# Kernel tuning notes

Hardware: AMD Instinct MI355X
Metric: run time of the kernel (lower is better)

Reference implementation:

```python
import jax, jax.numpy as jnp
import numpy as np

BS, SEQ, D_SSL = 256, 201, 1024
D1, D2 = 128, 64
N_NODE = SEQ // 3          # 67 nodes after max_pool1d(3)
N_POOL = int(N_NODE * 0.8) # 53 nodes after GraphPool(k=0.8)
EPS = 1e-5                 # BatchNorm eps (eval mode, running stats)


def setup_inputs() -> dict:
    key = jax.random.key(0)
    ks = jax.random.split(key, 16)
    def rn(k, shape, s=0.02):
        return jax.random.normal(k, shape, jnp.float32) * s
    return {
        "feat": jax.random.normal(ks[0], (BS, SEQ, D_SSL), jnp.float32),
        "W_ll": rn(ks[1], (D_SSL, D1)), "b_ll": jnp.zeros((D1,), jnp.float32),
        "bn1_g": jnp.ones((D1,), jnp.float32), "bn1_b": jnp.zeros((D1,), jnp.float32),
        "bn1_m": rn(ks[2], (D1,), 0.1),
        "bn1_v": jax.random.uniform(ks[3], (D1,), jnp.float32, 0.5, 1.5),
        "W_ap": rn(ks[4], (D1, D2)), "b_ap": jnp.zeros((D2,), jnp.float32),
        "att_w": rn(ks[5], (D2, 1), 0.1),
        "W_pa": rn(ks[6], (D1, D2)), "b_pa": jnp.zeros((D2,), jnp.float32),
        "W_pn": rn(ks[7], (D1, D2)), "b_pn": jnp.zeros((D2,), jnp.float32),
        "bn2_g": jnp.ones((D2,), jnp.float32), "bn2_b": jnp.zeros((D2,), jnp.float32),
        "bn2_m": rn(ks[8], (D2,), 0.1),
        "bn2_v": jax.random.uniform(ks[9], (D2,), jnp.float32, 0.5, 1.5),
        "W_pool": rn(ks[10], (D2, 1), 0.1), "b_pool": jnp.zeros((1,), jnp.float32),
        "W_proj": rn(ks[11], (D2, 1), 0.1), "b_proj": jnp.zeros((1,), jnp.float32),
        "W_node": rn(ks[12], (N_POOL, 2), 0.1), "b_node": jnp.zeros((2,), jnp.float32),
    }


def _bn(x, g, b, m, v):
    # eval-mode BatchNorm1d with running stats, applied per-channel (last dim)
    return (x - m) * jax.lax.rsqrt(v + EPS) * g + b


def reference(feat, W_ll, b_ll, bn1_g, bn1_b, bn1_m, bn1_v,
              W_ap, b_ap, att_w, W_pa, b_pa, W_pn, b_pn,
              bn2_g, bn2_b, bn2_m, bn2_v,
              W_pool, b_pool, W_proj, b_proj, W_node, b_node):
    # LL: (bs, seq, 1024) -> (bs, seq, 128)
    x = feat @ W_ll + b_ll
    # max_pool1d(kernel=3, stride=3) over the sequence dim -> (bs, 67, 128)
    x = x[:, :N_NODE * 3].reshape(BS, N_NODE, 3, D1).max(axis=2)
    x = jax.nn.selu(_bn(x, bn1_g, bn1_b, bn1_m, bn1_v))
    # --- GraphAttentionLayer ---
    pair = x[:, :, None, :] * x[:, None, :, :]            # (bs, n, n, 128) pairwise mul
    att = jnp.tanh(pair @ W_ap + b_ap) @ att_w            # (bs, n, n, 1)
    att = jax.nn.softmax(att, axis=-2)                    # softmax over second node axis
    x1 = jnp.einsum('bij,bjd->bid', att[..., 0], x) @ W_pa + b_pa
    x2 = x @ W_pn + b_pn
    h = jax.nn.selu(_bn(x1 + x2, bn2_g, bn2_b, bn2_m, bn2_v))  # (bs, n, 64)
    # --- GraphPool: top-k node selection ---
    scores = jax.nn.sigmoid(h @ W_pool + b_pool)          # (bs, n, 1)
    _, idx = jax.lax.top_k(scores[..., 0], N_POOL)        # (bs, 53)
    hs = jnp.take_along_axis(h * scores, idx[:, :, None], axis=1)  # (bs, 53, 64)
    # head: proj -> (bs, 53), proj_node -> (bs, 2)
    out = (hs @ W_proj + b_proj)[..., 0] @ W_node + b_node
    return out
```

## Files before the change

### kernel.cpp

```cpp
#include <hip/hip_runtime.h>
#include <stdint.h>
#include <math.h>


#define BS 256
#define SEQ 201
#define DS 1024
#define D1 128
#define D2 64
#define NN 67
#define NP 53
#define ROWS1 (BS * SEQ)
#define ROWS2 (BS * NN)

#define SELU_LAM 1.0507009873554805f
#define SELU_ALP 1.6732632423543772f

__device__ __forceinline__ float selu_f(float x) {
    return (x > 0.0f) ? SELU_LAM * x : SELU_LAM * (SELU_ALP * expm1f(x));
}

__device__ __forceinline__ float fc(float4 v, int k) {
    switch (k & 3) {
        case 0: return v.x;
        case 1: return v.y;
        case 2: return v.z;
        default: return v.w;
    }
}

__global__ __launch_bounds__(256) void k_pre(
    const float* __restrict__ Wll, const float* __restrict__ Wap,
    const float* __restrict__ v1, const float* __restrict__ v2,
    float* __restrict__ WllT, float* __restrict__ WapT,
    float* __restrict__ r1, float* __restrict__ r2)
{
    int t = blockIdx.x * 256 + threadIdx.x;
    if (t < 131072) {
        int c = t >> 10, k = t & 1023;
        WllT[t] = Wll[k * D1 + c];
    } else if (t < 139264) {
        int i = t - 131072; int c = i >> 7, d = i & 127;
        WapT[i] = Wap[d * D2 + c];
    } else if (t < 139392) {
        int d = t - 139264;
        r1[d] = 1.0f / sqrtf(v1[d] + 1e-5f);
    } else if (t < 139456) {
        int c = t - 139392;
        r2[c] = 1.0f / sqrtf(v2[c] + 1e-5f);
    }
}

__global__ __launch_bounds__(256) void k_gemm1(
    const float* __restrict__ A, const float* __restrict__ Bt,
    float* __restrict__ y)
{
    __shared__ __align__(16) float As[64 * 36];
    __shared__ __align__(16) float Bs[128 * 36];
    int tid = threadIdx.x;
    int row0 = blockIdx.x * 64;
    int ty = tid >> 4, tx = tid & 15;
    float acc[4][8];
#pragma unroll
    for (int r = 0; r < 4; ++r)
#pragma unroll
        for (int m = 0; m < 8; ++m) acc[r][m] = 0.0f;

    int si = tid >> 2, sk = (tid & 3) * 8;
    int bc = tid >> 1, bh = (tid & 1) * 16;
    const float* gA = A + (size_t)(row0 + si) * DS + sk;
    const float* gB = Bt + (size_t)bc * DS + bh;

    for (int k0 = 0; k0 < DS; k0 += 32) {
        float4 a0 = *(const float4*)(gA + k0);
        float4 a1 = *(const float4*)(gA + k0 + 4);
        float4 b0 = *(const float4*)(gB + k0);
        float4 b1 = *(const float4*)(gB + k0 + 4);
        float4 b2 = *(const float4*)(gB + k0 + 8);
        float4 b3 = *(const float4*)(gB + k0 + 12);
        __syncthreads();
        *(float4*)(As + si * 36 + sk)      = a0;
        *(float4*)(As + si * 36 + sk + 4)  = a1;
        *(float4*)(Bs + bc * 36 + bh)      = b0;
        *(float4*)(Bs + bc * 36 + bh + 4)  = b1;
        *(float4*)(Bs + bc * 36 + bh + 8)  = b2;
        *(float4*)(Bs + bc * 36 + bh + 12) = b3;
        __syncthreads();
#pragma unroll
        for (int k4 = 0; k4 < 8; ++k4) {
            float4 av[4], bv[8];
#pragma unroll
            for (int r = 0; r < 4; ++r)
                av[r] = *(const float4*)(As + (ty + 16 * r) * 36 + k4 * 4);
#pragma unroll
            for (int m = 0; m < 8; ++m)
                bv[m] = *(const float4*)(Bs + (tx + 16 * m) * 36 + k4 * 4);
#pragma unroll
            for (int r = 0; r < 4; ++r)
#pragma unroll
                for (int m = 0; m < 8; ++m) {
                    acc[r][m] += av[r].x * bv[m].x;
                    acc[r][m] += av[r].y * bv[m].y;
                    acc[r][m] += av[r].z * bv[m].z;
                    acc[r][m] += av[r].w * bv[m].w;
                }
        }
    }
#pragma unroll
    for (int r = 0; r < 4; ++r)
#pragma unroll
        for (int m = 0; m < 8; ++m)
            y[(size_t)(row0 + ty + 16 * r) * D1 + tx + 16 * m] = acc[r][m];
}

__global__ __launch_bounds__(256) void k_pool(
    const float* __restrict__ y, const float* __restrict__ bll,
    const float* __restrict__ g1, const float* __restrict__ b1,
    const float* __restrict__ m1, const float* __restrict__ r1,
    float* __restrict__ X)
{
    int t = blockIdx.x * 256 + threadIdx.x;
    int d = t & 127, rem = t >> 7;
    int n = rem % NN, b = rem / NN;
    size_t base = ((size_t)(b * SEQ + 3 * n)) * D1 + d;
    float bl = bll[d];
    float v0 = y[base] + bl;
    float v1v = y[base + D1] + bl;
    float v2v = y[base + 2 * D1] + bl;
    float v = fmaxf(fmaxf(v0, v1v), v2v);
    v = (v - m1[d]) * r1[d] * g1[d] + b1[d];
    X[(size_t)rem * D1 + d] = selu_f(v);
}

__global__ __launch_bounds__(256, 1) void k_attn(
    const float* __restrict__ X, const float* __restrict__ WapT,
    const float* __restrict__ bap, const float* __restrict__ attw,
    float* __restrict__ XA)
{
    __shared__ __align__(16) float Xs[80 * 132];
    __shared__ float e[80 * 85];
    int tid = threadIdx.x;
    int b = blockIdx.x;
    const float* Xb = X + (size_t)b * NN * D1;

#pragma unroll
    for (int q = 0; q < 40; ++q) {
        int t = q * 256 + tid;
        int r = t >> 7, d = t & 127;
        Xs[r * 132 + d] = (r < NN) ? Xb[(size_t)r * D1 + d] : 0.0f;
    }
    __syncthreads();

    int ti = tid >> 4, tj = tid & 15;

    float eacc[5][5];
#pragma unroll
    for (int a = 0; a < 5; ++a)
#pragma unroll
        for (int m = a; m < 5; ++m) eacc[a][m] = 0.0f;

    for (int cg = 0; cg < 16; ++cg) {
        float E[5][5][4];
#pragma unroll
        for (int a = 0; a < 5; ++a)
#pragma unroll
            for (int m = a; m < 5; ++m)
#pragma unroll
                for (int c = 0; c < 4; ++c) E[a][m][c] = 0.0f;

#pragma unroll 2
        for (int k4 = 0; k4 < 32; ++k4) {
            float4 xa[5], xv[5], w[4];
#pragma unroll
            for (int a = 0; a < 5; ++a)
                xa[a] = *(const float4*)(Xs + (ti + 16 * a) * 132 + k4 * 4);
#pragma unroll
            for (int m = 0; m < 5; ++m)
                xv[m] = *(const float4*)(Xs + (tj + 16 * m) * 132 + k4 * 4);
#pragma unroll
            for (int c = 0; c < 4; ++c)
                w[c] = *(const float4*)(WapT + (cg * 4 + c) * D1 + k4 * 4);
#pragma unroll
            for (int kk = 0; kk < 4; ++kk) {
#pragma unroll
                for (int a = 0; a < 5; ++a) {
                    float pa = fc(xa[a], kk);
#pragma unroll
                    for (int m = a; m < 5; ++m) {
                        float P = pa * fc(xv[m], kk);
                        E[a][m][0] += P * fc(w[0], kk);
                        E[a][m][1] += P * fc(w[1], kk);
                        E[a][m][2] += P * fc(w[2], kk);
                        E[a][m][3] += P * fc(w[3], kk);
                    }
                }
            }
        }
#pragma unroll
        for (int c = 0; c < 4; ++c) {
            float bc = bap[cg * 4 + c], ac = attw[cg * 4 + c];
#pragma unroll
            for (int a = 0; a < 5; ++a)
#pragma unroll
                for (int m = a; m < 5; ++m)
                    eacc[a][m] += tanhf(E[a][m][c] + bc) * ac;
        }
    }
#pragma unroll
    for (int a = 0; a < 5; ++a)
#pragma unroll
        for (int m = a; m < 5; ++m) {
            int i = ti + 16 * a, j = tj + 16 * m;
            e[i * 85 + j] = eacc[a][m];
            if (a < m) e[j * 85 + i] = eacc[a][m];
        }
    __syncthreads();

    if (tid < NN) {
        float* er = e + tid * 85;
        float mx = -1e30f;
        for (int j = 0; j < NN; ++j) mx = fmaxf(mx, er[j]);
        float sum = 0.0f;
        for (int j = 0; j < NN; ++j) { float p = expf(er[j] - mx); er[j] = p; sum += p; }
        float inv = 1.0f / sum;
        for (int j = 0; j < NN; ++j) er[j] *= inv;
    }
    __syncthreads();

    int d0 = tj * 8;
    float o[5][8];
#pragma unroll
    for (int a = 0; a < 5; ++a)
#pragma unroll
        for (int dd = 0; dd < 8; ++dd) o[a][dd] = 0.0f;
    for (int j = 0; j < NN; ++j) {
        float4 x0 = *(const float4*)(Xs + j * 132 + d0);
        float4 x1 = *(const float4*)(Xs + j * 132 + d0 + 4);
        float av[5];
#pragma unroll
        for (int a = 0; a < 5; ++a) av[a] = e[(ti + 16 * a) * 85 + j];
#pragma unroll
        for (int a = 0; a < 5; ++a) {
            o[a][0] += av[a] * x0.x; o[a][1] += av[a] * x0.y;
            o[a][2] += av[a] * x0.z; o[a][3] += av[a] * x0.w;
            o[a][4] += av[a] * x1.x; o[a][5] += av[a] * x1.y;
            o[a][6] += av[a] * x1.z; o[a][7] += av[a] * x1.w;
        }
    }
#pragma unroll
    for (int a = 0; a < 5; ++a) {
        int i = ti + 16 * a;
        if (i < NN) {
            float* dst = XA + (size_t)(b * NN + i) * D1 + d0;
            float4 s0, s1;
            s0.x = o[a][0]; s0.y = o[a][1]; s0.z = o[a][2]; s0.w = o[a][3];
            s1.x = o[a][4]; s1.y = o[a][5]; s1.z = o[a][6]; s1.w = o[a][7];
            *(float4*)(dst) = s0;
            *(float4*)(dst + 4) = s1;
        }
    }
}

__global__ __launch_bounds__(256) void k_gemm2(
    const float* __restrict__ XAg, const float* __restrict__ Xg,
    const float* __restrict__ Wpa, const float* __restrict__ Wpn,
    const float* __restrict__ bpa, const float* __restrict__ bpn,
    const float* __restrict__ g2, const float* __restrict__ b2,
    const float* __restrict__ m2, const float* __restrict__ r2,
    float* __restrict__ h)
{
    __shared__ __align__(16) float As[64 * 260];
    __shared__ __align__(16) float Ws[256 * 68];
    int tid = threadIdx.x;
    int row0 = blockIdx.x * 64;
#pragma unroll
    for (int q = 0; q < 16; ++q) {
        int e4 = q * 256 + tid;
        int r = e4 >> 6, k4 = (e4 & 63) * 4;
        float4 v;
        if (k4 < 128) v = *(const float4*)(XAg + (size_t)(row0 + r) * D1 + k4);
        else          v = *(const float4*)(Xg + (size_t)(row0 + r) * D1 + (k4 - 128));
        *(float4*)(As + r * 260 + k4) = v;
    }
#pragma unroll
    for (int q = 0; q < 16; ++q) {
        int e4 = q * 256 + tid;
        int k = e4 >> 4, c4 = (e4 & 15) * 4;
        float4 v;
        if (k < 128) v = *(const float4*)(Wpa + k * D2 + c4);
        else         v = *(const float4*)(Wpn + (k - 128) * D2 + c4);
        *(float4*)(Ws + k * 68 + c4) = v;
    }
    __syncthreads();
    int rl = tid >> 2, cq = (tid & 3) * 16;
    float acc[16];
#pragma unroll
    for (int m = 0; m < 16; ++m) acc[m] = 0.0f;
    for (int k = 0; k < 256; ++k) {
        float a = As[rl * 260 + k];
        float4 w0 = *(const float4*)(Ws + k * 68 + cq);
        float4 w1 = *(const float4*)(Ws + k * 68 + cq + 4);
        float4 w2 = *(const float4*)(Ws + k * 68 + cq + 8);
        float4 w3 = *(const float4*)(Ws + k * 68 + cq + 12);
        acc[0] += a * w0.x;  acc[1] += a * w0.y;  acc[2] += a * w0.z;  acc[3] += a * w0.w;
        acc[4] += a * w1.x;  acc[5] += a * w1.y;  acc[6] += a * w1.z;  acc[7] += a * w1.w;
        acc[8] += a * w2.x;  acc[9] += a * w2.y;  acc[10] += a * w2.z; acc[11] += a * w2.w;
        acc[12] += a * w3.x; acc[13] += a * w3.y; acc[14] += a * w3.z; acc[15] += a * w3.w;
    }
#pragma unroll
    for (int m = 0; m < 16; ++m) {
        int c = cq + m;
        float t = acc[m] + bpa[c] + bpn[c];
        t = (t - m2[c]) * r2[c] * g2[c] + b2[c];
        h[(size_t)(row0 + rl) * D2 + c] = selu_f(t);
    }
}

__global__ __launch_bounds__(64) void k_head(
    const float* __restrict__ h, const float* __restrict__ Wpool,
    const float* __restrict__ bpool, const float* __restrict__ Wproj,
    const float* __restrict__ bproj, const float* __restrict__ Wnode,
    const float* __restrict__ bnode, float* __restrict__ out)
{
    __shared__ float sc[NN], pv[NN], sel[NP];
    int lane = threadIdx.x, b = blockIdx.x;
    for (int j = lane; j < NN; j += 64) {
        const float* hr = h + (size_t)(b * NN + j) * D2;
        float z = 0.0f;
        for (int c = 0; c < D2; ++c) z += hr[c] * Wpool[c];
        z += bpool[0];
        float s = 1.0f / (1.0f + expf(-z));
        float q = 0.0f;
        for (int c = 0; c < D2; ++c) q += (hr[c] * s) * Wproj[c];
        q += bproj[0];
        sc[j] = s; pv[j] = q;
    }
    __syncthreads();
    for (int j = lane; j < NN; j += 64) {
        float sj = sc[j]; int rank = 0;
        for (int k = 0; k < NN; ++k) {
            float sk = sc[k];
            rank += (sk > sj) || (sk == sj && k < j);
        }
        if (rank < NP) sel[rank] = pv[j];
    }
    __syncthreads();
    if (lane < 2) {
        float o = 0.0f;
        for (int r = 0; r < NP; ++r) o += sel[r] * Wnode[r * 2 + lane];
        out[b * 2 + lane] = o + bnode[lane];
    }
}

extern "C" void kernel_launch(void* const* d_in, const int* in_sizes, int n_in,
                              void* d_out, int out_size, void* d_ws, size_t ws_size,
                              hipStream_t stream)
{
    const float* feat  = (const float*)d_in[0];
    const float* Wll   = (const float*)d_in[1];
    const float* bll   = (const float*)d_in[2];
    const float* g1    = (const float*)d_in[3];
    const float* b1    = (const float*)d_in[4];
    const float* m1    = (const float*)d_in[5];
    const float* v1    = (const float*)d_in[6];
    const float* Wap   = (const float*)d_in[7];
    const float* bap   = (const float*)d_in[8];
    const float* attw  = (const float*)d_in[9];
    const float* Wpa   = (const float*)d_in[10];
    const float* bpa   = (const float*)d_in[11];
    const float* Wpn   = (const float*)d_in[12];
    const float* bpn   = (const float*)d_in[13];
    const float* g2    = (const float*)d_in[14];
    const float* b2    = (const float*)d_in[15];
    const float* m2    = (const float*)d_in[16];
    const float* v2    = (const float*)d_in[17];
    const float* Wpool = (const float*)d_in[18];
    const float* bpool = (const float*)d_in[19];
    const float* Wproj = (const float*)d_in[20];
    const float* bproj = (const float*)d_in[21];
    const float* Wnode = (const float*)d_in[22];
    const float* bnode = (const float*)d_in[23];
    float* out = (float*)d_out;

    char* w = (char*)d_ws;
    float* y    = (float*)w; w += (size_t)ROWS1 * D1 * 4;
    float* X    = (float*)w; w += (size_t)ROWS2 * D1 * 4;
    float* XA   = (float*)w; w += (size_t)ROWS2 * D1 * 4;
    float* hbuf = (float*)w; w += (size_t)ROWS2 * D2 * 4;
    float* WllT = (float*)w; w += (size_t)128 * 1024 * 4;
    float* WapT = (float*)w; w += (size_t)64 * 128 * 4;
    float* r1   = (float*)w; w += 128 * 4;
    float* r2   = (float*)w; w += 64 * 4;

    hipLaunchKernelGGL(k_pre,   dim3(545),  dim3(256), 0, stream,
                       Wll, Wap, v1, v2, WllT, WapT, r1, r2);
    hipLaunchKernelGGL(k_gemm1, dim3(804),  dim3(256), 0, stream, feat, WllT, y);
    hipLaunchKernelGGL(k_pool,  dim3(8576), dim3(256), 0, stream,
                       y, bll, g1, b1, m1, r1, X);
    hipLaunchKernelGGL(k_attn,  dim3(256),  dim3(256), 0, stream,
                       X, WapT, bap, attw, XA);
    hipLaunchKernelGGL(k_gemm2, dim3(268),  dim3(256), 0, stream,
                       XA, X, Wpa, Wpn, bpa, bpn, g2, b2, m2, r2, hbuf);
    hipLaunchKernelGGL(k_head,  dim3(256),  dim3(64),  0, stream,
                       hbuf, Wpool, bpool, Wproj, bproj, Wnode, bnode, out);
}
```

Measured before the change: 1.008 ms.

## Split attention over channel halves across blocks and enlarge gemm1 row tile

The attention-score kernel is split into two kernels. The first computes partial scores over half of the 64 hidden channels per block, giving 512 blocks instead of 256, and writes them to scratch that reuses the y buffer. The second sums the two partials, applies the softmax and does the aggregation. Separately, gemm1 now tiles 128 rows per block with an 8x8 per-thread accumulator, doubling A-tile reuse, at the cost of higher register pressure and half as many blocks.

```diff
diff --git a/kernel.cpp b/kernel.cpp
--- a/kernel.cpp
+++ b/kernel.cpp
@@ -55,48 +55,49 @@
     const float* __restrict__ A, const float* __restrict__ Bt,
     float* __restrict__ y)
 {
-    __shared__ __align__(16) float As[64 * 36];
+    __shared__ __align__(16) float As[128 * 36];
     __shared__ __align__(16) float Bs[128 * 36];
     int tid = threadIdx.x;
-    int row0 = blockIdx.x * 64;
+    int row0 = blockIdx.x * 128;
     int ty = tid >> 4, tx = tid & 15;
-    float acc[4][8];
-#pragma unroll
-    for (int r = 0; r < 4; ++r)
+    float acc[8][8];
+#pragma unroll
+    for (int r = 0; r < 8; ++r)
 #pragma unroll
         for (int m = 0; m < 8; ++m) acc[r][m] = 0.0f;
 
-    int si = tid >> 2, sk = (tid & 3) * 8;
-    int bc = tid >> 1, bh = (tid & 1) * 16;
-    const float* gA = A + (size_t)(row0 + si) * DS + sk;
-    const float* gB = Bt + (size_t)bc * DS + bh;
+    int lr = tid >> 1, lc = (tid & 1) * 16;
+    const float* gA = A + (size_t)(row0 + lr) * DS + lc;
+    const float* gB = Bt + (size_t)lr * DS + lc;
+    float* wa = As + lr * 36 + lc;
+    float* wb = Bs + lr * 36 + lc;
 
     for (int k0 = 0; k0 < DS; k0 += 32) {
         float4 a0 = *(const float4*)(gA + k0);
         float4 a1 = *(const float4*)(gA + k0 + 4);
+        float4 a2 = *(const float4*)(gA + k0 + 8);
+        float4 a3 = *(const float4*)(gA + k0 + 12);
         float4 b0 = *(const float4*)(gB + k0);
         float4 b1 = *(const float4*)(gB + k0 + 4);
         float4 b2 = *(const float4*)(gB + k0 + 8);
         float4 b3 = *(const float4*)(gB + k0 + 12);
         __syncthreads();
-        *(float4*)(As + si * 36 + sk)      = a0;
-        *(float4*)(As + si * 36 + sk + 4)  = a1;
-        *(float4*)(Bs + bc * 36 + bh)      = b0;
-        *(float4*)(Bs + bc * 36 + bh + 4)  = b1;
-        *(float4*)(Bs + bc * 36 + bh + 8)  = b2;
-        *(float4*)(Bs + bc * 36 + bh + 12) = b3;
+        *(float4*)(wa)      = a0; *(float4*)(wa + 4)  = a1;
+        *(float4*)(wa + 8)  = a2; *(float4*)(wa + 12) = a3;
+        *(float4*)(wb)      = b0; *(float4*)(wb + 4)  = b1;
+        *(float4*)(wb + 8)  = b2; *(float4*)(wb + 12) = b3;
         __syncthreads();
 #pragma unroll
         for (int k4 = 0; k4 < 8; ++k4) {
-            float4 av[4], bv[8];
-#pragma unroll
-            for (int r = 0; r < 4; ++r)
+            float4 av[8], bv[8];
+#pragma unroll
+            for (int r = 0; r < 8; ++r)
                 av[r] = *(const float4*)(As + (ty + 16 * r) * 36 + k4 * 4);
 #pragma unroll
             for (int m = 0; m < 8; ++m)
                 bv[m] = *(const float4*)(Bs + (tx + 16 * m) * 36 + k4 * 4);
 #pragma unroll
-            for (int r = 0; r < 4; ++r)
+            for (int r = 0; r < 8; ++r)
 #pragma unroll
                 for (int m = 0; m < 8; ++m) {
                     acc[r][m] += av[r].x * bv[m].x;
@@ -107,7 +108,7 @@
         }
     }
 #pragma unroll
-    for (int r = 0; r < 4; ++r)
+    for (int r = 0; r < 8; ++r)
 #pragma unroll
         for (int m = 0; m < 8; ++m)
             y[(size_t)(row0 + ty + 16 * r) * D1 + tx + 16 * m] = acc[r][m];
@@ -132,15 +133,15 @@
     X[(size_t)rem * D1 + d] = selu_f(v);
 }
 
-__global__ __launch_bounds__(256, 1) void k_attn(
+__global__ __launch_bounds__(256) void k_attn1(
     const float* __restrict__ X, const float* __restrict__ WapT,
     const float* __restrict__ bap, const float* __restrict__ attw,
-    float* __restrict__ XA)
+    float* __restrict__ epart)
 {
     __shared__ __align__(16) float Xs[80 * 132];
-    __shared__ float e[80 * 85];
     int tid = threadIdx.x;
-    int b = blockIdx.x;
+    int blk = blockIdx.x;
+    int b = blk >> 1, z = blk & 1;
     const float* Xb = X + (size_t)b * NN * D1;
 
 #pragma unroll
@@ -159,7 +160,7 @@
 #pragma unroll
         for (int m = a; m < 5; ++m) eacc[a][m] = 0.0f;
 
-    for (int cg = 0; cg < 16; ++cg) {
+    for (int cg = z * 8; cg < z * 8 + 8; ++cg) {
         float E[5][5][4];
 #pragma unroll
         for (int a = 0; a < 5; ++a)
@@ -206,14 +207,40 @@
                     eacc[a][m] += tanhf(E[a][m][c] + bc) * ac;
         }
     }
+
+    float* ep = epart + (size_t)blk * 6400;
 #pragma unroll
     for (int a = 0; a < 5; ++a)
 #pragma unroll
         for (int m = a; m < 5; ++m) {
             int i = ti + 16 * a, j = tj + 16 * m;
-            e[i * 85 + j] = eacc[a][m];
-            if (a < m) e[j * 85 + i] = eacc[a][m];
-        }
+            ep[i * 80 + j] = eacc[a][m];
+            if (a < m) ep[j * 80 + i] = eacc[a][m];
+        }
+}
+
+__global__ __launch_bounds__(256) void k_attn2(
+    const float* __restrict__ X, const float* __restrict__ epart,
+    float* __restrict__ XA)
+{
+    __shared__ __align__(16) float Xs[80 * 132];
+    __shared__ float e[80 * 85];
+    int tid = threadIdx.x;
+    int b = blockIdx.x;
+    const float* Xb = X + (size_t)b * NN * D1;
+
+#pragma unroll
+    for (int q = 0; q < 40; ++q) {
+        int t = q * 256 + tid;
+        int r = t >> 7, d = t & 127;
+        Xs[r * 132 + d] = (r < NN) ? Xb[(size_t)r * D1 + d] : 0.0f;
+    }
+    const float* e0 = epart + (size_t)(b * 2) * 6400;
+    const float* e1 = e0 + 6400;
+    for (int t = tid; t < 6400; t += 256) {
+        int i = t / 80, j = t - i * 80;
+        e[i * 85 + j] = e0[t] + e1[t];
+    }
     __syncthreads();
 
     if (tid < NN) {
@@ -227,6 +254,7 @@
     }
     __syncthreads();
 
+    int ti = tid >> 4, tj = tid & 15;
     int d0 = tj * 8;
     float o[5][8];
 #pragma unroll
@@ -391,14 +419,17 @@
     float* WapT = (float*)w; w += (size_t)64 * 128 * 4;
     float* r1   = (float*)w; w += 128 * 4;
     float* r2   = (float*)w; w += 64 * 4;
+    float* epart = y;
 
     hipLaunchKernelGGL(k_pre,   dim3(545),  dim3(256), 0, stream,
                        Wll, Wap, v1, v2, WllT, WapT, r1, r2);
-    hipLaunchKernelGGL(k_gemm1, dim3(804),  dim3(256), 0, stream, feat, WllT, y);
+    hipLaunchKernelGGL(k_gemm1, dim3(402),  dim3(256), 0, stream, feat, WllT, y);
     hipLaunchKernelGGL(k_pool,  dim3(8576), dim3(256), 0, stream,
                        y, bll, g1, b1, m1, r1, X);
-    hipLaunchKernelGGL(k_attn,  dim3(256),  dim3(256), 0, stream,
-                       X, WapT, bap, attw, XA);
+    hipLaunchKernelGGL(k_attn1, dim3(512),  dim3(256), 0, stream,
+                       X, WapT, bap, attw, epart);
+    hipLaunchKernelGGL(k_attn2, dim3(256),  dim3(256), 0, stream,
+                       X, epart, XA);
     hipLaunchKernelGGL(k_gemm2, dim3(268),  dim3(256), 0, stream,
                        XA, X, Wpa, Wpn, bpa, bpn, g2, b2, m2, r2, hbuf);
     hipLaunchKernelGGL(k_head,  dim3(256),  dim3(64),  0, stream,
```

Result: faster. 810.8 us (-19.6%).
